# Kernel tuning notes

Measured on AMD Instinct MI355X. Metric: run time of the kernel, lower is better.

Reference implementation:

```python
import jax, jax.numpy as jnp
import numpy as np

K = 27  # num_neighs, hardcoded in module
EPS = 1e-5


def knn_idx(x, k):
    # x: (B, N, 3) -> (B, N, k) indices of k nearest neighbors (self included)
    xx = jnp.sum(x * x, axis=-1)                      # (B, N)
    inner = jnp.einsum('bnd,bmd->bnm', x, x)          # (B, N, N)
    d = 2.0 * inner - xx[:, :, None] - xx[:, None, :] # negative sq dist
    return jax.lax.top_k(d, k)[1]


def graph_feature(f, idx):
    # f: (B, N, C), idx: (B, N, k) -> (B, N, k, 2C) = [neigh - center, center]
    neigh = jax.vmap(lambda fb, ib: fb[ib])(f, idx)   # (B, N, k, C)
    center = jnp.broadcast_to(f[:, :, None, :], neigh.shape)
    return jnp.concatenate([neigh - center, center], axis=-1)


def bn_lrelu(y, g, b, axes):
    m = jnp.mean(y, axis=axes, keepdims=True)
    v = jnp.var(y, axis=axes, keepdims=True)
    y = (y - m) * jax.lax.rsqrt(v + EPS) * g + b
    return jnp.where(y >= 0, y, 0.2 * y)


def edge_conv(f, idx, W, g, b):
    # f: (B, N, C) -> (B, N, C_out); 1x1 conv over (B, 2C, N, k) + BN + LeakyReLU + max over k
    h = graph_feature(f, idx)                         # (B, N, k, 2C)
    y = jnp.einsum('bnkc,oc->bnko', h, W)             # (B, N, k, C_out)
    y = bn_lrelu(y, g, b, axes=(0, 1, 2))
    return jnp.max(y, axis=2)                         # (B, N, C_out)


def setup_inputs() -> dict:
    key = jax.random.key(0)
    ks = jax.random.split(key, 8)
    B, N, latent = 2, 2048, 256
    x = jax.random.normal(ks[0], (B, N, 3), dtype=jnp.float32)
    chans = [(6, 96), (192, 192), (384, 384), (768, 768)]
    inp = {'x': x}
    for i, (cin, cout) in enumerate(chans):
        inp[f'W{i}'] = jax.random.normal(ks[1 + i], (cout, cin), dtype=jnp.float32) * np.sqrt(2.0 / cin).astype(np.float32)
        inp[f'g{i}'] = jnp.ones((cout,), dtype=jnp.float32)
        inp[f'b{i}'] = jnp.zeros((cout,), dtype=jnp.float32)
    inp['W4'] = jax.random.normal(ks[5], (latent, 1440), dtype=jnp.float32) * np.sqrt(2.0 / 1440).astype(np.float32)
    inp['g4'] = jnp.ones((latent,), dtype=jnp.float32)
    inp['b4'] = jnp.zeros((latent,), dtype=jnp.float32)
    return inp


def reference(x, W0, g0, b0, W1, g1, b1, W2, g2, b2, W3, g3, b3, W4, g4, b4):
    # x: (B, N, 3)
    idx = knn_idx(x, K)                               # (B, N, K), fixed for all layers (only_true_neighs=True)
    outs = []
    f = x
    for (W, g, b) in ((W0, g0, b0), (W1, g1, b1), (W2, g2, b2), (W3, g3, b3)):
        f = edge_conv(f, idx, W, g, b)
        outs.append(f)
    h = jnp.concatenate(outs, axis=-1)                # (B, N, 1440)
    y = jnp.einsum('bnc,oc->bno', h, W4)              # (B, N, latent)
    feats = bn_lrelu(y, g4, b4, axes=(0, 1))          # features_per_point (B, N, latent)
    global_feat = jnp.max(feats, axis=1)              # (B, latent)
    return global_feat, feats
```

## Files before the change

kernel.cpp:

```cpp
#include <hip/hip_runtime.h>
#include <hip/hip_bf16.h>

#define BATCH 2
#define NPB   2048
#define NPTS  4096
#define KNB   27
#define FCATC 1440
#define CSTRIDE 1696
#define NSLOT 32
#define PBATCH 4

#define WOFF_L1 0
#define WOFF_L2 36864
#define WOFF_L3 184320
#define WOFF_F  774144
#define WTOTAL  1142784

typedef __hip_bfloat16 bf16;
typedef __attribute__((ext_vector_type(8))) short short8;
typedef __attribute__((ext_vector_type(4))) float f32x4;
typedef __attribute__((ext_vector_type(2))) short s16x2;

__device__ __forceinline__ float b2f(bf16 v) { return __bfloat162float(v); }

__device__ __forceinline__ void split_bf16(float v, bf16& h, bf16& l) {
    h = __float2bfloat16(v);
    l = __float2bfloat16(v - b2f(h));
}

__device__ __forceinline__ float ldin(const void* p, size_t i, int f32) {
    return f32 ? ((const float*)p)[i] : b2f(((const bf16*)p)[i]);
}

__device__ __forceinline__ void gl16(const bf16* g, bf16* l) {
    __builtin_amdgcn_global_load_lds(
        (const __attribute__((address_space(1))) unsigned int*)g,
        (__attribute__((address_space(3))) unsigned int*)l,
        16, 0, 0);
}

__global__ void k_init(const void* __restrict__ x, int* __restrict__ flag,
                       float* __restrict__ xf, float* __restrict__ slots) {
    if (blockIdx.x < 424) {
        slots[blockIdx.x * 256 + threadIdx.x] = 0.f;
        return;
    }
    __shared__ int s;
    if (threadIdx.x == 0) s = 0;
    __syncthreads();
    const bf16* xb = (const bf16*)x;
    int local = 0;
    for (int i = threadIdx.x; i < NPTS * 3; i += 256) {
        float v = b2f(xb[i]);
        if (!(fabsf(v) < 1e4f)) local = 1;
    }
    if (local) s = 1;
    __syncthreads();
    int f32 = s;
    if (threadIdx.x == 0) flag[0] = f32;
    for (int i = threadIdx.x; i < NPTS * 3; i += 256) xf[i] = ldin(x, i, f32);
}

__global__ __launch_bounds__(256) void k_knn(const float* __restrict__ x, int* __restrict__ idx) {
    __shared__ uint hist4[4][260];
    __shared__ uint hist[256];
    __shared__ uint tkey[NPB];
    __shared__ int  tix[NPB];
    __shared__ uint s_phigh;
    __shared__ int  s_rem, s_outcnt, s_tiecnt;

    int bn = blockIdx.x, b = bn >> 11, n = bn & (NPB - 1);
    int tid = threadIdx.x;
    int wv = tid >> 6;
    const float* xb = x + (size_t)b * NPB * 3;
    float cx = xb[n * 3 + 0], cy = xb[n * 3 + 1], cz = xb[n * 3 + 2];
    float cc = cx * cx + cy * cy + cz * cz;

    uint u[8];
    #pragma unroll
    for (int j = 0; j < 8; j++) {
        int m = j * 256 + tid;
        float mx = xb[m * 3 + 0], my = xb[m * 3 + 1], mz = xb[m * 3 + 2];
        float d = 2.f * (cx * mx + cy * my + cz * mz) - cc - (mx * mx + my * my + mz * mz);
        uint s = __float_as_uint(d);
        u[j] = (s & 0x80000000u) ? ~s : (s | 0x80000000u);
    }
    if (tid == 0) { s_phigh = 0; s_rem = KNB; s_outcnt = 0; s_tiecnt = 0; }

    for (int pass = 0; pass < 2; pass++) {
        int shift = 24 - pass * 8;
        hist[tid] = 0;
        for (int i = tid; i < 4 * 260; i += 256) ((uint*)hist4)[i] = 0;
        __syncthreads();
        uint phigh = s_phigh;
        #pragma unroll
        for (int j = 0; j < 8; j++) {
            bool in = (pass == 0) || ((u[j] >> (shift + 8)) == phigh);
            if (in) atomicAdd(&hist4[wv][(u[j] >> shift) & 0xFFu], 1u);
        }
        __syncthreads();
        hist[tid] = hist4[0][tid] + hist4[1][tid] + hist4[2][tid] + hist4[3][tid];
        __syncthreads();
        if (tid < 64) {
            int L = tid;
            uint c0 = hist[L * 4 + 0], c1 = hist[L * 4 + 1], c2 = hist[L * 4 + 2], c3 = hist[L * 4 + 3];
            uint s = c0 + c1 + c2 + c3;
            uint acc = s;
            #pragma unroll
            for (int off = 1; off < 64; off <<= 1) {
                uint t = __shfl_down(acc, off);
                if (L + off < 64) acc += t;
            }
            uint excl = acc - s;
            int rem = s_rem;
            if ((int)excl < rem && (int)acc >= rem) {
                uint cs[4] = { c0, c1, c2, c3 };
                uint cum = excl;
                int bsel = 0; uint hb = 0;
                #pragma unroll
                for (int q = 3; q >= 0; q--) {
                    if ((int)cum < rem && (int)(cum + cs[q]) >= rem && hb == 0u && bsel == 0) {
                        bsel = L * 4 + q; hb = cs[q]; cum += cs[q];
                    } else if (bsel == 0 && hb == 0u) {
                        cum += cs[q];
                    }
                }
                int strictlyAbove = (int)(cum - hb);
                s_rem = rem - strictlyAbove;
                s_phigh = (phigh << 8) | (uint)bsel;
            }
        }
        __syncthreads();
    }

    uint T16 = s_phigh;
    #pragma unroll
    for (int j = 0; j < 8; j++) {
        int m = j * 256 + tid;
        uint hi = u[j] >> 16;
        if (hi > T16) {
            int p = atomicAdd(&s_outcnt, 1);
            idx[bn * KNB + p] = b * NPB + m;
        } else if (hi == T16) {
            int p = atomicAdd(&s_tiecnt, 1);
            tkey[p] = u[j];
            tix[p] = m;
        }
    }
    __syncthreads();
    int outcnt = s_outcnt, rem = s_rem, tiecnt = s_tiecnt;
    if (tiecnt == rem) {
        if (tid < rem) idx[bn * KNB + outcnt + tid] = b * NPB + tix[tid];
    } else if (tid == 0) {
        for (int t = 0; t < rem; t++) {
            int bi = 0;
            for (int q = 1; q < tiecnt; q++)
                if (tkey[q] > tkey[bi] || (tkey[q] == tkey[bi] && tix[q] < tix[bi])) bi = q;
            idx[bn * KNB + outcnt + t] = b * NPB + tix[bi];
            tkey[bi] = 0; tix[bi] = 0x7fffffff;
        }
    }
}

__global__ void k_l0(const float* __restrict__ xf, const void* __restrict__ W,
                     const int* __restrict__ flag, bf16* __restrict__ Ub, float* __restrict__ Vf) {
    int i = blockIdx.x * 256 + threadIdx.x;
    if (i >= NPTS * 192) return;
    int bn = i / 192, o = i % 192;
    int f32 = flag[0];
    float x0 = xf[bn * 3 + 0], x1 = xf[bn * 3 + 1], x2 = xf[bn * 3 + 2];
    if (o < 96) {
        float r = x0 * ldin(W, o * 6 + 0, f32) + x1 * ldin(W, o * 6 + 1, f32) + x2 * ldin(W, o * 6 + 2, f32);
        Ub[(size_t)bn * 96 + o] = __float2bfloat16(r);
    } else {
        int oo = o - 96;
        float w0 = ldin(W, oo * 6 + 3, f32) - ldin(W, oo * 6 + 0, f32);
        float w1 = ldin(W, oo * 6 + 4, f32) - ldin(W, oo * 6 + 1, f32);
        float w2 = ldin(W, oo * 6 + 5, f32) - ldin(W, oo * 6 + 2, f32);
        Vf[(size_t)bn * 96 + oo] = x0 * w0 + x1 * w1 + x2 * w2;
    }
}

__global__ void k_wt_all(const void* __restrict__ W1, const void* __restrict__ W2,
                         const void* __restrict__ W3, const void* __restrict__ W4,
                         const int* __restrict__ flag,
                         bf16* __restrict__ Wh, bf16* __restrict__ Wl) {
    int i = blockIdx.x * 256 + threadIdx.x;
    if (i >= WTOTAL) return;
    int f32 = flag[0];
    float w;
    if (i < WOFF_L2) {
        int row = i / 96, c = i % 96;
        w = (row < 192) ? ldin(W1, (size_t)row * 192 + c, f32)
                        : ldin(W1, (size_t)(row - 192) * 192 + 96 + c, f32)
                          - ldin(W1, (size_t)(row - 192) * 192 + c, f32);
    } else if (i < WOFF_L3) {
        int j = i - WOFF_L2;
        int row = j / 192, c = j % 192;
        w = (row < 384) ? ldin(W2, (size_t)row * 384 + c, f32)
                        : ldin(W2, (size_t)(row - 384) * 384 + 192 + c, f32)
                          - ldin(W2, (size_t)(row - 384) * 384 + c, f32);
    } else if (i < WOFF_F) {
        int j = i - WOFF_L3;
        int row = j / 384, c = j % 384;
        w = (row < 768) ? ldin(W3, (size_t)row * 768 + c, f32)
                        : ldin(W3, (size_t)(row - 768) * 768 + 384 + c, f32)
                          - ldin(W3, (size_t)(row - 768) * 768 + c, f32);
    } else {
        int j = i - WOFF_F;
        w = ldin(W4, j, f32);
    }
    bf16 h, l; split_bf16(w, h, l);
    Wh[i] = h; Wl[i] = l;
}

template<int TILE>
__global__ __launch_bounds__(256) void k_gemm_mfma(const bf16* __restrict__ Ah, const bf16* __restrict__ Al,
                                                   int lda, int aoff,
                                                   const bf16* __restrict__ Bh, const bf16* __restrict__ Bl,
                                                   int K, bf16* __restrict__ Cu, float* __restrict__ Cv,
                                                   int Cosplit, int ldc, int ksz, int zstride) {
    constexpr int FR  = TILE / 32;
    constexpr int ISS = TILE / 64;
    constexpr int MY  = (NPTS / TILE) / 8;
    __shared__ __align__(16) bf16 Ash[TILE][32];
    __shared__ __align__(16) bf16 Asl[TILE][32];
    __shared__ __align__(16) bf16 Bsh[TILE][32];
    __shared__ __align__(16) bf16 Bsl[TILE][32];
    int tid = threadIdx.x;
    int wave = tid >> 6, lane = tid & 63;
    int wm = wave >> 1, wn = wave & 1;
    int quad = lane >> 4, l15 = lane & 15;
    int Lxy = blockIdx.y * gridDim.x + blockIdx.x;
    int stripe = Lxy & 7;
    int w = Lxy >> 3;
    int mb = stripe * MY + (w & (MY - 1));
    int nb = w / MY;
    int m0 = mb * TILE, n0 = nb * TILE;
    int kbase = blockIdx.z * ksz;
    float* Cz = Cv + (size_t)blockIdx.z * zstride;

    int cc = wave * 64 + lane;

    f32x4 acc[FR][FR] = {};
    for (int k0 = kbase; k0 < kbase + ksz; k0 += 32) {
        #pragma unroll
        for (int i = 0; i < ISS; i++) {
            int c = cc + i * 256;
            int rr = c >> 2, cl = (c & 3) << 3;
            size_t ga = (size_t)(m0 + rr) * lda + aoff + k0 + cl;
            size_t gb = (size_t)(n0 + rr) * K + k0 + cl;
            bf16* dst = (bf16*)nullptr;
            gl16(Ah + ga, &Ash[0][0] + wave * 512 + i * 2048);
            gl16(Al + ga, &Asl[0][0] + wave * 512 + i * 2048);
            gl16(Bh + gb, &Bsh[0][0] + wave * 512 + i * 2048);
            gl16(Bl + gb, &Bsl[0][0] + wave * 512 + i * 2048);
            (void)dst;
        }
        __syncthreads();
        short8 ahf[FR], alf[FR], bhf[FR], blf[FR];
        #pragma unroll
        for (int mt = 0; mt < FR; mt++) {
            int rr = wm * (TILE / 2) + mt * 16 + l15;
            ahf[mt] = *(const short8*)&Ash[rr][quad * 8];
            alf[mt] = *(const short8*)&Asl[rr][quad * 8];
        }
        #pragma unroll
        for (int nt = 0; nt < FR; nt++) {
            int rr = wn * (TILE / 2) + nt * 16 + l15;
            bhf[nt] = *(const short8*)&Bsh[rr][quad * 8];
            blf[nt] = *(const short8*)&Bsl[rr][quad * 8];
        }
        __syncthreads();
        #pragma unroll
        for (int mt = 0; mt < FR; mt++) {
            #pragma unroll
            for (int nt = 0; nt < FR; nt++) {
                acc[mt][nt] = __builtin_amdgcn_mfma_f32_16x16x32_bf16(ahf[mt], blf[nt], acc[mt][nt], 0, 0, 0);
                acc[mt][nt] = __builtin_amdgcn_mfma_f32_16x16x32_bf16(alf[mt], bhf[nt], acc[mt][nt], 0, 0, 0);
                acc[mt][nt] = __builtin_amdgcn_mfma_f32_16x16x32_bf16(ahf[mt], bhf[nt], acc[mt][nt], 0, 0, 0);
            }
        }
    }
    #pragma unroll
    for (int mt = 0; mt < FR; mt++) {
        #pragma unroll
        for (int nt = 0; nt < FR; nt++) {
            int col = n0 + wn * (TILE / 2) + nt * 16 + l15;
            #pragma unroll
            for (int i = 0; i < 4; i++) {
                int row = m0 + wm * (TILE / 2) + mt * 16 + quad * 4 + i;
                if (Cosplit > 0) {
                    if (col < Cosplit) Cu[(size_t)row * Cosplit + col] = __float2bfloat16(acc[mt][nt][i]);
                    else               Cv[(size_t)row * Cosplit + col - Cosplit] = acc[mt][nt][i];
                } else {
                    Cz[(size_t)row * ldc + col] = acc[mt][nt][i];
                }
            }
        }
    }
}

__global__ __launch_bounds__(256) void k_gather(const bf16* __restrict__ Ub, float* __restrict__ Vf,
                                                const int* __restrict__ idx,
                                                bf16* __restrict__ fch, bf16* __restrict__ fcl,
                                                float* __restrict__ ssum, float* __restrict__ ssq,
                                                int Co, int out_off) {
    __shared__ int srow[PBATCH * KNB];
    int tid = threadIdx.x;
    int L = blockIdx.y * gridDim.x + blockIdx.x;
    int batch = L & 1;
    int w = L >> 1;
    int pg = batch * 512 + (w & 511);
    int chunk = w >> 9;
    int p0 = pg * PBATCH;
    if (tid < PBATCH * KNB) srow[tid] = idx[p0 * KNB + tid] * Co;
    __syncthreads();
    int P = Co >> 1;
    int op = chunk * 256 + tid;
    if (op >= P) return;
    int o = op * 2;
    int slot = pg & (NSLOT - 1);
    float s0 = 0.f, s1 = 0.f, q0 = 0.f, q1 = 0.f;
    #pragma unroll 1
    for (int p = 0; p < PBATCH; p++) {
        int bn = p0 + p;
        float2 vv = *(const float2*)&Vf[(size_t)bn * Co + o];
        float ymax0 = -INFINITY, ymax1 = -INFINITY, ymin0 = INFINITY, ymin1 = INFINITY;
        #pragma unroll
        for (int k = 0; k < KNB; k++) {
            uint wb = *(const uint*)&Ub[(size_t)srow[p * KNB + k] + o];
            float y0 = __uint_as_float(wb << 16) + vv.x;
            float y1 = __uint_as_float(wb & 0xffff0000u) + vv.y;
            ymax0 = fmaxf(ymax0, y0); ymin0 = fminf(ymin0, y0); s0 += y0; q0 += y0 * y0;
            ymax1 = fmaxf(ymax1, y1); ymin1 = fminf(ymin1, y1); s1 += y1; q1 += y1 * y1;
        }
        size_t fi = (size_t)bn * FCATC + out_off + o;
        bf16 hh[2], ll[2];
        split_bf16(ymax0, hh[0], ll[0]);
        split_bf16(ymax1, hh[1], ll[1]);
        *(s16x2*)&fch[fi] = *(const s16x2*)hh;
        *(s16x2*)&fcl[fi] = *(const s16x2*)ll;
        *(float2*)&Vf[(size_t)bn * Co + o] = make_float2(ymin0, ymin1);
    }
    atomicAdd(&ssum[slot * CSTRIDE + o + 0], s0);
    atomicAdd(&ssum[slot * CSTRIDE + o + 1], s1);
    atomicAdd(&ssq [slot * CSTRIDE + o + 0], q0);
    atomicAdd(&ssq [slot * CSTRIDE + o + 1], q1);
}

__global__ void k_scaleshift(const float* __restrict__ ssum, const float* __restrict__ ssq,
                             const void* __restrict__ g, const void* __restrict__ bb,
                             const int* __restrict__ flag,
                             float* __restrict__ scale, float* __restrict__ shift, int Co, float invcnt) {
    int o = blockIdx.x * 256 + threadIdx.x;
    if (o >= Co) return;
    int f32 = flag[0];
    float s = 0.f, q = 0.f;
    for (int c = 0; c < NSLOT; c++) { s += ssum[c * CSTRIDE + o]; q += ssq[c * CSTRIDE + o]; }
    float mean = s * invcnt;
    float var = q * invcnt - mean * mean;
    float sc = ldin(g, o, f32) * rsqrtf(var + 1e-5f);
    scale[o] = sc;
    shift[o] = ldin(bb, o, f32) - mean * sc;
}

__global__ __launch_bounds__(256) void k_apply(const float* __restrict__ Vf,
                                               const float* __restrict__ scale, const float* __restrict__ shift,
                                               bf16* __restrict__ fch, bf16* __restrict__ fcl,
                                               int Co, int out_off) {
    int bn = blockIdx.x;
    for (int o = threadIdx.x; o < Co; o += 256) {
        float sc = scale[o], sh = shift[o];
        size_t fi = (size_t)bn * FCATC + out_off + o;
        float y = (sc >= 0.f) ? (b2f(fch[fi]) + b2f(fcl[fi]))
                              : Vf[(size_t)bn * Co + o];
        float z = sc * y + sh;
        z = (z >= 0.f) ? z : 0.2f * z;
        bf16 h, l; split_bf16(z, h, l);
        fch[fi] = h; fcl[fi] = l;
    }
}

__global__ void k_stats_final(const float* __restrict__ part, float* __restrict__ Y,
                              float* __restrict__ ssum, float* __restrict__ ssq) {
    int o = threadIdx.x;
    int p0 = blockIdx.x * 16;
    int slot = blockIdx.x & (NSLOT - 1);
    const size_t PL = (size_t)NPTS * 256;
    float s = 0, q = 0;
    for (int p = 0; p < 16; p++) {
        size_t i = (size_t)(p0 + p) * 256 + o;
        float y = part[i] + part[i + PL] + part[i + 2 * PL] + part[i + 3 * PL] + part[i + 4 * PL];
        Y[i] = y;
        s += y; q += y * y;
    }
    atomicAdd(&ssum[slot * CSTRIDE + o], s);
    atomicAdd(&ssq [slot * CSTRIDE + o], q);
}

__global__ void k_feats(const float* __restrict__ Y, const float* __restrict__ ssum,
                        const float* __restrict__ ssq, const void* __restrict__ g,
                        const void* __restrict__ bb, const int* __restrict__ flag,
                        void* __restrict__ out, float* __restrict__ partial) {
    int o = threadIdx.x;
    int chunk = blockIdx.x;
    int bn0 = chunk * 32;
    int f32 = flag[0];
    float s = 0.f, q = 0.f;
    for (int c = 0; c < NSLOT; c++) { s += ssum[c * CSTRIDE + o]; q += ssq[c * CSTRIDE + o]; }
    float mean = s * (1.f / (float)NPTS);
    float var = q * (1.f / (float)NPTS) - mean * mean;
    float sc = ldin(g, o, f32) * rsqrtf(var + 1e-5f);
    float sh = ldin(bb, o, f32) - mean * sc;
    float best = -INFINITY;
    for (int i = 0; i < 32; i++) {
        int bn = bn0 + i;
        float z = sc * Y[(size_t)bn * 256 + o] + sh;
        z = (z >= 0.f) ? z : 0.2f * z;
        size_t oi = (size_t)BATCH * 256 + (size_t)bn * 256 + o;
        if (f32) ((float*)out)[oi] = z;
        else     ((bf16*)out)[oi] = __float2bfloat16(z);
        best = fmaxf(best, z);
    }
    partial[chunk * 256 + o] = best;
}

__global__ void k_gmax(const float* __restrict__ partial, void* __restrict__ out, const int* __restrict__ flag) {
    int o = threadIdx.x;
    int b = blockIdx.x;
    float best = -INFINITY;
    for (int c = 0; c < 64; c++) best = fmaxf(best, partial[(b * 64 + c) * 256 + o]);
    if (flag[0]) ((float*)out)[b * 256 + o] = best;
    else         ((bf16*)out)[b * 256 + o] = __float2bfloat16(best);
}

extern "C" void kernel_launch(void* const* d_in, const int* in_sizes, int n_in,
                              void* d_out, int out_size, void* d_ws, size_t ws_size,
                              hipStream_t stream) {
    const void* x = d_in[0];

    char* ws = (char*)d_ws;
    int*   idx    = (int*)  (ws + 0);
    bf16*  Ub     = (bf16*) (ws + 442368);
    float* Vf     = (float*)(ws + 6733824);
    float* part   = (float*)(ws + 442368);
    bf16*  fch    = (bf16*) (ws + 25608192);
    bf16*  fcl    = (bf16*) (ws + 37404672);
    float* Y4     = (float*)(ws + 49201152);
    bf16*  Whall  = (bf16*) (ws + 53395456);
    bf16*  Wlall  = (bf16*) (ws + 55681024);
    float* slots  = (float*)(ws + 57966592);
    float* ssum   = slots;
    float* ssq    = slots + NSLOT * CSTRIDE;
    float* scales = (float*)(ws + 58400768);
    float* shifts = (float*)(ws + 58407552);
    float* partial= (float*)(ws + 442368);
    float* xf     = (float*)(ws + 58479872);
    int*   flag   = (int*)  (ws + 58529024);

    const int Cin[4]  = {3, 96, 192, 384};
    const int Co[4]   = {96, 192, 384, 768};
    const int ooff[4] = {0, 96, 288, 672};
    const int soff[5] = {0, 96, 288, 672, 1440};
    const int woff[4] = {0, WOFF_L1, WOFF_L2, WOFF_L3};

    hipLaunchKernelGGL(k_init, dim3(425), dim3(256), 0, stream, x, flag, xf, slots);
    hipLaunchKernelGGL(k_knn, dim3(NPTS), dim3(256), 0, stream, xf, idx);
    hipLaunchKernelGGL(k_wt_all, dim3((WTOTAL + 255) / 256), dim3(256), 0, stream,
                       d_in[4], d_in[7], d_in[10], d_in[13], flag, Whall, Wlall);

    const float invcnt_edge = 1.f / (float)(NPTS * KNB);
    for (int L = 0; L < 4; L++) {
        const void* g  = d_in[2 + 3 * L];
        const void* bb = d_in[3 + 3 * L];
        int N2 = 2 * Co[L];
        if (L == 0) {
            hipLaunchKernelGGL(k_l0, dim3((NPTS * 192 + 255) / 256), dim3(256), 0, stream,
                               xf, d_in[1], flag, Ub, Vf);
        } else if (L < 3) {
            hipLaunchKernelGGL(k_gemm_mfma<64>, dim3(N2 / 64, NPTS / 64, 1), dim3(256), 0, stream,
                               fch, fcl, FCATC, ooff[L - 1], Whall + woff[L], Wlall + woff[L], Cin[L],
                               Ub, Vf, Co[L], 0, Cin[L], 0);
        } else {
            hipLaunchKernelGGL(k_gemm_mfma<128>, dim3(N2 / 128, NPTS / 128, 1), dim3(256), 0, stream,
                               fch, fcl, FCATC, ooff[L - 1], Whall + woff[L], Wlall + woff[L], Cin[L],
                               Ub, Vf, Co[L], 0, Cin[L], 0);
        }
        int nchunks = ((Co[L] / 2) + 255) / 256;
        hipLaunchKernelGGL(k_gather, dim3(NPTS / PBATCH, nchunks), dim3(256), 0, stream,
                           Ub, Vf, idx, fch, fcl, ssum + soff[L], ssq + soff[L], Co[L], ooff[L]);
        hipLaunchKernelGGL(k_scaleshift, dim3((Co[L] + 255) / 256), dim3(256), 0, stream,
                           ssum + soff[L], ssq + soff[L], g, bb, flag,
                           scales + soff[L], shifts + soff[L], Co[L], invcnt_edge);
        hipLaunchKernelGGL(k_apply, dim3(NPTS), dim3(256), 0, stream,
                           Vf, scales + soff[L], shifts + soff[L], fch, fcl, Co[L], ooff[L]);
    }

    hipLaunchKernelGGL(k_gemm_mfma<128>, dim3(256 / 128, NPTS / 128, 5), dim3(256), 0, stream,
                       fch, fcl, FCATC, 0, Whall + WOFF_F, Wlall + WOFF_F, FCATC,
                       (bf16*)nullptr, part, 0, 256, 288, NPTS * 256);
    hipLaunchKernelGGL(k_stats_final, dim3(256), dim3(256), 0, stream, part, Y4, ssum + soff[4], ssq + soff[4]);
    hipLaunchKernelGGL(k_feats, dim3(128), dim3(256), 0, stream, Y4, ssum + soff[4], ssq + soff[4],
                       d_in[14], d_in[15], flag, d_out, partial);
    hipLaunchKernelGGL(k_gmax, dim3(BATCH), dim3(256), 0, stream, partial, d_out, flag);
}
```

Baseline: 328.6 us.

## Double-buffer LDS tiles and XOR-swizzle columns in split-bf16 MFMA GEMM

Measured after the change: 322.2 us. About the same (-1.9%).

```diff
diff --git a/kernel.cpp b/kernel.cpp
--- a/kernel.cpp
+++ b/kernel.cpp
@@ -223,10 +223,10 @@
     constexpr int FR  = TILE / 32;
     constexpr int ISS = TILE / 64;
     constexpr int MY  = (NPTS / TILE) / 8;
-    __shared__ __align__(16) bf16 Ash[TILE][32];
-    __shared__ __align__(16) bf16 Asl[TILE][32];
-    __shared__ __align__(16) bf16 Bsh[TILE][32];
-    __shared__ __align__(16) bf16 Bsl[TILE][32];
+    __shared__ __align__(16) bf16 Ash[2][TILE][32];
+    __shared__ __align__(16) bf16 Asl[2][TILE][32];
+    __shared__ __align__(16) bf16 Bsh[2][TILE][32];
+    __shared__ __align__(16) bf16 Bsl[2][TILE][32];
     int tid = threadIdx.x;
     int wave = tid >> 6, lane = tid & 63;
     int wm = wave >> 1, wn = wave & 1;
@@ -240,38 +240,52 @@
     int kbase = blockIdx.z * ksz;
     float* Cz = Cv + (size_t)blockIdx.z * zstride;
 
-    int cc = wave * 64 + lane;
-
+    int rr_s[ISS], cl_s[ISS];
+    #pragma unroll
+    for (int i = 0; i < ISS; i++) {
+        int c = wave * 64 + lane + i * 256;
+        rr_s[i] = c >> 2;
+        cl_s[i] = (((c & 3) ^ ((c >> 3) & 3)) << 3);
+    }
+
+    auto STAGE = [&](int buf, int k0) {
+        #pragma unroll
+        for (int i = 0; i < ISS; i++) {
+            size_t ga = (size_t)(m0 + rr_s[i]) * lda + aoff + k0 + cl_s[i];
+            size_t gb = (size_t)(n0 + rr_s[i]) * K + k0 + cl_s[i];
+            bf16* la  = &Ash[buf][0][0] + wave * 512 + i * 2048;
+            bf16* lal = &Asl[buf][0][0] + wave * 512 + i * 2048;
+            bf16* lb  = &Bsh[buf][0][0] + wave * 512 + i * 2048;
+            bf16* lbl = &Bsl[buf][0][0] + wave * 512 + i * 2048;
+            gl16(Ah + ga, la);
+            gl16(Al + ga, lal);
+            gl16(Bh + gb, lb);
+            gl16(Bl + gb, lbl);
+        }
+    };
+
+    int nsteps = ksz >> 5;
     f32x4 acc[FR][FR] = {};
-    for (int k0 = kbase; k0 < kbase + ksz; k0 += 32) {
-        #pragma unroll
-        for (int i = 0; i < ISS; i++) {
-            int c = cc + i * 256;
-            int rr = c >> 2, cl = (c & 3) << 3;
-            size_t ga = (size_t)(m0 + rr) * lda + aoff + k0 + cl;
-            size_t gb = (size_t)(n0 + rr) * K + k0 + cl;
-            bf16* dst = (bf16*)nullptr;
-            gl16(Ah + ga, &Ash[0][0] + wave * 512 + i * 2048);
-            gl16(Al + ga, &Asl[0][0] + wave * 512 + i * 2048);
-            gl16(Bh + gb, &Bsh[0][0] + wave * 512 + i * 2048);
-            gl16(Bl + gb, &Bsl[0][0] + wave * 512 + i * 2048);
-            (void)dst;
-        }
-        __syncthreads();
+    STAGE(0, kbase);
+    __syncthreads();
+    int cur = 0;
+    for (int t = 0; t < nsteps; t++) {
+        if (t + 1 < nsteps) STAGE(cur ^ 1, kbase + ((t + 1) << 5));
         short8 ahf[FR], alf[FR], bhf[FR], blf[FR];
         #pragma unroll
         for (int mt = 0; mt < FR; mt++) {
             int rr = wm * (TILE / 2) + mt * 16 + l15;
-            ahf[mt] = *(const short8*)&Ash[rr][quad * 8];
-            alf[mt] = *(const short8*)&Asl[rr][quad * 8];
+            int qs = (quad ^ ((rr >> 1) & 3)) * 8;
+            ahf[mt] = *(const short8*)&Ash[cur][rr][qs];
+            alf[mt] = *(const short8*)&Asl[cur][rr][qs];
         }
         #pragma unroll
         for (int nt = 0; nt < FR; nt++) {
             int rr = wn * (TILE / 2) + nt * 16 + l15;
-            bhf[nt] = *(const short8*)&Bsh[rr][quad * 8];
-            blf[nt] = *(const short8*)&Bsl[rr][quad * 8];
-        }
-        __syncthreads();
+            int qs = (quad ^ ((rr >> 1) & 3)) * 8;
+            bhf[nt] = *(const short8*)&Bsh[cur][rr][qs];
+            blf[nt] = *(const short8*)&Bsl[cur][rr][qs];
+        }
         #pragma unroll
         for (int mt = 0; mt < FR; mt++) {
             #pragma unroll
@@ -281,6 +295,8 @@
                 acc[mt][nt] = __builtin_amdgcn_mfma_f32_16x16x32_bf16(ahf[mt], bhf[nt], acc[mt][nt], 0, 0, 0);
             }
         }
+        __syncthreads();
+        cur ^= 1;
     }
     #pragma unroll
     for (int mt = 0; mt < FR; mt++) {
```
